# Optimization experiments

Measured on AMD Instinct MI355X. Metric: run time of the kernel, lower is better.

## Reference

```python
import jax, jax.numpy as jnp
import numpy as np

N_NODES = 100000
N_EDGES = 3200000


def setup_inputs() -> dict:
    key = jax.random.key(0)
    ks = jax.random.split(key, 12)
    x = jax.random.normal(ks[0], (N_NODES, 34), dtype=jnp.float32)
    edge_index = jax.random.randint(ks[1], (2, N_EDGES), 0, N_NODES, dtype=jnp.int64)
    def lin(k, fin, fout):
        s = 1.0 / np.sqrt(fin)
        kw, kb = jax.random.split(k)
        W = jax.random.uniform(kw, (fin, fout), jnp.float32, -s, s)
        b = jax.random.uniform(kb, (fout,), jnp.float32, -s, s)
        return W, b
    W1, b1 = lin(ks[2], 34, 64)
    W2, b2 = lin(ks[3], 64, 32)
    W3, b3 = lin(ks[4], 32, 16)
    W4, b4 = lin(ks[5], 16, 8)
    Wc, bc = lin(ks[6], 8, 2)
    return {"x": x, "edge_index": edge_index,
            "W1": W1, "b1": b1, "W2": W2, "b2": b2,
            "W3": W3, "b3": b3, "W4": W4, "b4": b4,
            "Wc": Wc, "bc": bc}


def _gcn_norm(edge_index, n_nodes):
    # PyG GCNConv: add self-loops, symmetric normalization D^-1/2 (A+I) D^-1/2
    loop = jnp.arange(n_nodes, dtype=edge_index.dtype)
    src = jnp.concatenate([edge_index[0], loop])  # [E+N]
    dst = jnp.concatenate([edge_index[1], loop])
    deg = jax.ops.segment_sum(jnp.ones_like(dst, dtype=jnp.float32), dst,
                              num_segments=n_nodes)
    dinv = jnp.where(deg > 0, jax.lax.rsqrt(deg), 0.0)
    norm = dinv[src] * dinv[dst]  # [E+N]
    return src, dst, norm


def _gcn_conv(h, W, b, src, dst, norm, n_nodes):
    h = h @ W                                    # [N, Fout] small GEMM
    msg = h[src] * norm[:, None]                 # gather + scale
    out = jax.ops.segment_sum(msg, dst, num_segments=n_nodes)  # scatter-add
    return out + b


def reference(x, edge_index, W1, b1, W2, b2, W3, b3, W4, b4, Wc, bc):
    n = x.shape[0]
    src, dst, norm = _gcn_norm(edge_index, n)
    h = jnp.tanh(_gcn_conv(x, W1, b1, src, dst, norm, n))
    h = jnp.tanh(_gcn_conv(h, W2, b2, src, dst, norm, n))
    h = jnp.tanh(_gcn_conv(h, W3, b3, src, dst, norm, n))
    h = jnp.tanh(_gcn_conv(h, W4, b4, src, dst, norm, n))
    out = h @ Wc + bc
    return (out, h)
```

## Files before the change

### kernel.cpp

```cpp
#include <hip/hip_runtime.h>
#include <math.h>

#define N_NODES 100000
#define BSHIFT 8
#define BNODES 256
#define NB ((N_NODES + BNODES - 1) / BNODES)
#define CHUNK 8192


typedef float f32x2 __attribute__((ext_vector_type(2)));

__device__ __forceinline__ unsigned short f2bf(float x) {
    unsigned u = __float_as_uint(x);
    u += 0x7FFFu + ((u >> 16) & 1u);
    return (unsigned short)(u >> 16);
}
__device__ __forceinline__ unsigned pack2(float a, float b) {
    return (unsigned)f2bf(a) | ((unsigned)f2bf(b) << 16);
}
__device__ __forceinline__ float bflo(unsigned u) { return __uint_as_float(u << 16); }
__device__ __forceinline__ float bfhi(unsigned u) { return __uint_as_float(u & 0xFFFF0000u); }

__device__ __forceinline__ int nt_ld(const int* p) { return __builtin_nontemporal_load(p); }
__device__ __forceinline__ void nt_st2(float* p, float a, float b) {
    f32x2 v; v.x = a; v.y = b;
    __builtin_nontemporal_store(v, (f32x2*)p);
}
__device__ __forceinline__ void nt_st(float* p, float a) { __builtin_nontemporal_store(a, p); }


__global__ __launch_bounds__(256) void bucket_count(const int* __restrict__ dst,
                                                    int* __restrict__ bucketCount, int E) {
    __shared__ int hist[NB];
    for (int i = threadIdx.x; i < NB; i += 256) hist[i] = 0;
    __syncthreads();
    int i = blockIdx.x * blockDim.x + threadIdx.x;
    int stride = gridDim.x * blockDim.x;
    for (int e = i; e < E; e += stride)
        atomicAdd(&hist[nt_ld(dst + e) >> BSHIFT], 1);
    __syncthreads();
    for (int i2 = threadIdx.x; i2 < NB; i2 += 256) {
        int c = hist[i2];
        if (c) atomicAdd(&bucketCount[i2], c);
    }
}


__global__ __launch_bounds__(512) void bucket_scan(const int* __restrict__ bucketCount,
                                                   int* __restrict__ bucketOff,
                                                   int* __restrict__ bucketCursor, int E) {
    __shared__ int sh[512];
    int t = threadIdx.x;
    int v = (t < NB) ? bucketCount[t] : 0;
    sh[t] = v;
    __syncthreads();
    for (int d = 1; d < 512; d <<= 1) {
        int u = (t >= d) ? sh[t - d] : 0;
        __syncthreads();
        sh[t] += u;
        __syncthreads();
    }
    if (t < NB) { bucketOff[t] = sh[t] - v; bucketCursor[t] = sh[t] - v; }
    if (t == 0) bucketOff[NB] = E;
}


__global__ __launch_bounds__(256) void bucket_fill(const int* __restrict__ src,
                                                   const int* __restrict__ dst,
                                                   int* __restrict__ bucketCursor,
                                                   unsigned int* __restrict__ binned, int E) {
    __shared__ int hist[NB];
    __shared__ int base[NB];
    __shared__ int lcur[NB];
    __shared__ unsigned int recs[CHUNK];
    __shared__ unsigned short bkt[CHUNK];
    int t = threadIdx.x;
    for (int i = t; i < NB; i += 256) { hist[i] = 0; lcur[i] = 0; }
    __syncthreads();
    int cbase = blockIdx.x * CHUNK;
#pragma unroll
    for (int j = 0; j < CHUNK / 256; ++j) {
        int slot = t + j * 256;
        int e = cbase + slot;
        if (e < E) {
            int s = nt_ld(src + e);
            int d = nt_ld(dst + e);
            recs[slot] = (unsigned)s | ((unsigned)(d & (BNODES - 1)) << 17);
            int b = d >> BSHIFT;
            bkt[slot] = (unsigned short)b;
            atomicAdd(&hist[b], 1);
        } else {
            bkt[slot] = 0xFFFF;
        }
    }
    __syncthreads();
    for (int i = t; i < NB; i += 256) {
        int c = hist[i];
        base[i] = c ? atomicAdd(&bucketCursor[i], c) : 0;
    }
    __syncthreads();
#pragma unroll
    for (int j = 0; j < CHUNK / 256; ++j) {
        int slot = t + j * 256;
        unsigned short b = bkt[slot];
        if (b != 0xFFFF) {
            int pos = base[b] + atomicAdd(&lcur[b], 1);
            binned[pos] = recs[slot];
        }
    }
}


__global__ __launch_bounds__(256) void node_off_sort(const unsigned int* __restrict__ binned,
                                                     const int* __restrict__ bucketOff,
                                                     int* __restrict__ off,
                                                     float* __restrict__ dinv,
                                                     int* __restrict__ srcs, int n, int E) {
    __shared__ int hist[BNODES];
    __shared__ int sh[BNODES];
    __shared__ int lcur[BNODES];
    int t = threadIdx.x;
    int b = blockIdx.x;
    hist[t] = 0;
    __syncthreads();
    int rb = bucketOff[b], re = bucketOff[b + 1];
    for (int e = rb + t; e < re; e += 256)
        atomicAdd(&hist[(binned[e] >> 17) & 255], 1);
    __syncthreads();
    int v = hist[t];
    sh[t] = v;
    __syncthreads();
    for (int d = 1; d < 256; d <<= 1) {
        int u = (t >= d) ? sh[t - d] : 0;
        __syncthreads();
        sh[t] += u;
        __syncthreads();
    }
    int base = rb + sh[t] - v;
    lcur[t] = base;
    int g = b * BNODES + t;
    if (g < n) {
        off[g] = base;
        dinv[g] = rsqrtf((float)v + 1.0f);
    }
    if (b == NB - 1 && t == 0) off[n] = E;
    __syncthreads();
    for (int e = rb + t; e < re; e += 256) {
        unsigned int r = binned[e];
        int pos = atomicAdd(&lcur[(r >> 17) & 255], 1);
        srcs[pos] = (int)(r & 0x1FFFF);
    }
}


__global__ void x_pack(const float* __restrict__ x, const float* __restrict__ dinv,
                       unsigned* __restrict__ xm, unsigned* __restrict__ xt, int n) {
    int i = blockIdx.x * blockDim.x + threadIdx.x;
    if (i >= n) return;
    float dv = dinv[i];
    const float2* xr = (const float2*)(x + (size_t)i * 34);
    unsigned* om = xm + (size_t)i * 16;
#pragma unroll
    for (int j = 0; j < 16; ++j) { float2 v = xr[j]; om[j] = pack2(dv * v.x, dv * v.y); }
    float2 v = xr[16];
    xt[i] = pack2(dv * v.x, dv * v.y);
}


__global__ __launch_bounds__(256) void gather_x_bf16(const int* __restrict__ off,
        const int* __restrict__ srcs, const unsigned* __restrict__ xm,
        const unsigned* __restrict__ xt, const float* __restrict__ dinv,
        float* __restrict__ aggx, int n) {
    int g = blockIdx.x * 16 + (threadIdx.x >> 4);
    int f = threadIdx.x & 15;
    if (g >= n) return;
    int rb = off[g], re = off[g + 1];
    unsigned ug = xm[(size_t)g * 16 + f];
    float a0 = bflo(ug), a1 = bfhi(ug);
    float a2 = 0.f, a3 = 0.f;
    if (f == 0) { unsigned tt = xt[g]; a2 = bflo(tt); a3 = bfhi(tt); }
    int e = rb;
    for (; e + 8 <= re; e += 8) {
        int s0 = nt_ld(srcs + e),     s1 = nt_ld(srcs + e + 1);
        int s2 = nt_ld(srcs + e + 2), s3 = nt_ld(srcs + e + 3);
        int s4 = nt_ld(srcs + e + 4), s5 = nt_ld(srcs + e + 5);
        int s6 = nt_ld(srcs + e + 6), s7 = nt_ld(srcs + e + 7);
        unsigned u0 = xm[(size_t)s0 * 16 + f], u1 = xm[(size_t)s1 * 16 + f];
        unsigned u2 = xm[(size_t)s2 * 16 + f], u3 = xm[(size_t)s3 * 16 + f];
        unsigned u4 = xm[(size_t)s4 * 16 + f], u5 = xm[(size_t)s5 * 16 + f];
        unsigned u6 = xm[(size_t)s6 * 16 + f], u7 = xm[(size_t)s7 * 16 + f];
        a0 += bflo(u0); a1 += bfhi(u0); a0 += bflo(u1); a1 += bfhi(u1);
        a0 += bflo(u2); a1 += bfhi(u2); a0 += bflo(u3); a1 += bfhi(u3);
        a0 += bflo(u4); a1 += bfhi(u4); a0 += bflo(u5); a1 += bfhi(u5);
        a0 += bflo(u6); a1 += bfhi(u6); a0 += bflo(u7); a1 += bfhi(u7);
        if (f == 0) {
            unsigned t0 = xt[s0], t1 = xt[s1], t2 = xt[s2], t3 = xt[s3];
            unsigned t4 = xt[s4], t5 = xt[s5], t6 = xt[s6], t7 = xt[s7];
            a2 += bflo(t0); a3 += bfhi(t0); a2 += bflo(t1); a3 += bfhi(t1);
            a2 += bflo(t2); a3 += bfhi(t2); a2 += bflo(t3); a3 += bfhi(t3);
            a2 += bflo(t4); a3 += bfhi(t4); a2 += bflo(t5); a3 += bfhi(t5);
            a2 += bflo(t6); a3 += bfhi(t6); a2 += bflo(t7); a3 += bfhi(t7);
        }
    }
    for (; e < re; ++e) {
        int s = nt_ld(srcs + e);
        unsigned u = xm[(size_t)s * 16 + f];
        a0 += bflo(u); a1 += bfhi(u);
        if (f == 0) { unsigned tt = xt[s]; a2 += bflo(tt); a3 += bfhi(tt); }
    }
    float dv = dinv[g];
    nt_st2(aggx + (size_t)g * 34 + 2 * f, dv * a0, dv * a1);
    if (f == 0) nt_st2(aggx + (size_t)g * 34 + 32, dv * a2, dv * a3);
}


template<int FIN, int FOUT>
__global__ void gemm_tanh(const float* __restrict__ h, const float* __restrict__ W,
                          const float* __restrict__ bias, float* __restrict__ o, int n) {
    __shared__ float sW[FIN * FOUT];
    for (int i = threadIdx.x; i < FIN * FOUT; i += blockDim.x) sW[i] = W[i];
    __syncthreads();
    constexpr int ROWS = 256 / FOUT;
    int f = threadIdx.x % FOUT;
    int r = threadIdx.x / FOUT;
    int row = blockIdx.x * ROWS + r;
    if (row >= n) return;
    const float* hr = h + (size_t)row * FIN;
    float acc = 0.f;
#pragma unroll
    for (int k = 0; k < FIN; ++k) acc = fmaf(hr[k], sW[k * FOUT + f], acc);
    nt_st(o + (size_t)row * FOUT + f, tanhf(acc + bias[f]));
}


template<int FIN, int FOUT>
__global__ void gemm_pack(const float* __restrict__ h, const float* __restrict__ W,
                          const float* __restrict__ dinv, unsigned* __restrict__ linh, int n) {
    __shared__ float sW[FIN * FOUT];
    for (int i = threadIdx.x; i < FIN * FOUT; i += blockDim.x) sW[i] = W[i];
    __syncthreads();
    constexpr int NL = FOUT / 2;
    constexpr int ROWS = 256 / NL;
    int f = threadIdx.x % NL;
    int r = threadIdx.x / NL;
    int row = blockIdx.x * ROWS + r;
    if (row >= n) return;
    const float* hr = h + (size_t)row * FIN;
    float a0 = 0.f, a1 = 0.f;
#pragma unroll
    for (int k = 0; k < FIN; ++k) {
        float v = hr[k];
        a0 = fmaf(v, sW[k * FOUT + 2 * f], a0);
        a1 = fmaf(v, sW[k * FOUT + 2 * f + 1], a1);
    }
    float dv = dinv[row];
    linh[(size_t)row * NL + f] = pack2(dv * a0, dv * a1);
}


template<int F, bool CLS>
__global__ __launch_bounds__(256) void gather_bf16(const int* __restrict__ off,
        const int* __restrict__ srcs, const unsigned* __restrict__ linh,
        const float* __restrict__ dinv, const float* __restrict__ bias,
        float* __restrict__ h, const float* __restrict__ Wc,
        const float* __restrict__ bc, float* __restrict__ out, int n) {
    constexpr int NL = F / 2;
    int g = blockIdx.x * (256 / NL) + threadIdx.x / NL;
    int f = threadIdx.x % NL;
    if (g >= n) return;
    int rb = off[g], re = off[g + 1];
    unsigned ug = linh[(size_t)g * NL + f];
    float a0 = bflo(ug), a1 = bfhi(ug);
    int e = rb;
    for (; e + 8 <= re; e += 8) {
        int s0 = nt_ld(srcs + e),     s1 = nt_ld(srcs + e + 1);
        int s2 = nt_ld(srcs + e + 2), s3 = nt_ld(srcs + e + 3);
        int s4 = nt_ld(srcs + e + 4), s5 = nt_ld(srcs + e + 5);
        int s6 = nt_ld(srcs + e + 6), s7 = nt_ld(srcs + e + 7);
        unsigned u0 = linh[(size_t)s0 * NL + f], u1 = linh[(size_t)s1 * NL + f];
        unsigned u2 = linh[(size_t)s2 * NL + f], u3 = linh[(size_t)s3 * NL + f];
        unsigned u4 = linh[(size_t)s4 * NL + f], u5 = linh[(size_t)s5 * NL + f];
        unsigned u6 = linh[(size_t)s6 * NL + f], u7 = linh[(size_t)s7 * NL + f];
        a0 += bflo(u0); a1 += bfhi(u0); a0 += bflo(u1); a1 += bfhi(u1);
        a0 += bflo(u2); a1 += bfhi(u2); a0 += bflo(u3); a1 += bfhi(u3);
        a0 += bflo(u4); a1 += bfhi(u4); a0 += bflo(u5); a1 += bfhi(u5);
        a0 += bflo(u6); a1 += bfhi(u6); a0 += bflo(u7); a1 += bfhi(u7);
    }
    for (; e < re; ++e) {
        int s = nt_ld(srcs + e);
        unsigned u = linh[(size_t)s * NL + f];
        a0 += bflo(u); a1 += bfhi(u);
    }
    float dv = dinv[g];
    a0 = tanhf(fmaf(dv, a0, bias[2 * f]));
    a1 = tanhf(fmaf(dv, a1, bias[2 * f + 1]));
    nt_st2(h + (size_t)g * F + 2 * f, a0, a1);
    if (CLS) {
        float p0 = a0 * Wc[4 * f]     + a1 * Wc[4 * f + 2];
        float p1 = a0 * Wc[4 * f + 1] + a1 * Wc[4 * f + 3];
        p0 += __shfl_xor(p0, 1); p1 += __shfl_xor(p1, 1);
        p0 += __shfl_xor(p0, 2); p1 += __shfl_xor(p1, 2);
        if (f == 0) {
            out[(size_t)g * 2]     = p0 + bc[0];
            out[(size_t)g * 2 + 1] = p1 + bc[1];
        }
    }
}


static inline char* alignp(char* p) {
    return (char*)(((uintptr_t)p + 15) & ~(uintptr_t)15);
}

extern "C" void kernel_launch(void* const* d_in, const int* in_sizes, int n_in,
                              void* d_out, int out_size, void* d_ws, size_t ws_size,
                              hipStream_t stream) {
    const float* x  = (const float*)d_in[0];
    const int*   ei = (const int*)d_in[1];
    const float* W1 = (const float*)d_in[2];  const float* b1 = (const float*)d_in[3];
    const float* W2 = (const float*)d_in[4];  const float* b2 = (const float*)d_in[5];
    const float* W3 = (const float*)d_in[6];  const float* b3 = (const float*)d_in[7];
    const float* W4 = (const float*)d_in[8];  const float* b4 = (const float*)d_in[9];
    const float* Wc = (const float*)d_in[10]; const float* bc = (const float*)d_in[11];

    float* out  = (float*)d_out;
    float* hout = out + (size_t)2 * N_NODES;

    const int n = N_NODES;
    const int E = in_sizes[1] / 2;
    const int* src = ei;
    const int* dst = ei + E;

    char* w = (char*)d_ws;
    float*        dinv         = (float*)w;        w = alignp(w + (size_t)n * 4);
    int*          bucketCount  = (int*)w;          w = alignp(w + (size_t)NB * 4);
    int*          bucketOff    = (int*)w;          w = alignp(w + (size_t)(NB + 1) * 4);
    int*          bucketCursor = (int*)w;          w = alignp(w + (size_t)NB * 4);
    int*          off          = (int*)w;          w = alignp(w + (size_t)(n + 1) * 4);
    unsigned int* binned       = (unsigned int*)w; w = alignp(w + (size_t)E * 4);
    int*          srcs         = (int*)w;          w = alignp(w + (size_t)E * 4);
    unsigned int* xm           = (unsigned int*)w; w = alignp(w + (size_t)n * 16 * 4);
    unsigned int* xt           = (unsigned int*)w; w = alignp(w + (size_t)n * 4);
    float*        aggx         = (float*)w;        w = alignp(w + (size_t)n * 34 * 4);
    float*        hA           = (float*)w;        w = alignp(w + (size_t)n * 64 * 4);
    float*        hB           = (float*)w;        w = alignp(w + (size_t)n * 32 * 4);
    unsigned int* linh         = (unsigned int*)w; w = alignp(w + (size_t)n * 16 * 4);

    hipMemsetAsync(bucketCount, 0, NB * sizeof(int), stream);
    bucket_count<<<1024, 256, 0, stream>>>(dst, bucketCount, E);
    bucket_scan<<<1, 512, 0, stream>>>(bucketCount, bucketOff, bucketCursor, E);
    bucket_fill<<<(E + CHUNK - 1) / CHUNK, 256, 0, stream>>>(src, dst, bucketCursor, binned, E);
    node_off_sort<<<NB, 256, 0, stream>>>(binned, bucketOff, off, dinv, srcs, n, E);
    x_pack<<<(n + 255) / 256, 256, 0, stream>>>(x, dinv, xm, xt, n);

    gather_x_bf16<<<(n + 15) / 16, 256, 0, stream>>>(off, srcs, xm, xt, dinv, aggx, n);
    gemm_tanh<34, 64><<<(n + 3) / 4, 256, 0, stream>>>(aggx, W1, b1, hA, n);

    gemm_pack<64, 32><<<(n + 15) / 16, 256, 0, stream>>>(hA, W2, dinv, linh, n);
    gather_bf16<32, false><<<(n + 15) / 16, 256, 0, stream>>>(off, srcs, linh, dinv, b2, hB,
                                                              Wc, bc, out, n);

    gemm_pack<32, 16><<<(n + 31) / 32, 256, 0, stream>>>(hB, W3, dinv, linh, n);
    gather_bf16<16, false><<<(n + 31) / 32, 256, 0, stream>>>(off, srcs, linh, dinv, b3, hA,
                                                              Wc, bc, out, n);

    gemm_pack<16, 8><<<(n + 63) / 64, 256, 0, stream>>>(hA, W4, dinv, linh, n);
    gather_bf16<8, true><<<(n + 63) / 64, 256, 0, stream>>>(off, srcs, linh, dinv, b4, hout,
                                                            Wc, bc, out, n);
}
```

Measured before the change: 510.9 us.

## Fuse layer GEMMs into neighboring gather kernels to cut intermediate round-trips

Merges the layer-1 GEMM+tanh with the layer-2 projection into one kernel that keeps the 64-wide hidden row in shared memory. Folds the layer-3 and layer-4 projections into the preceding gather kernels using wavefront shuffles to reduce across lanes. This removes three launches and the fp32 intermediate writes and reads of hA and hB. The cost is a 16-way shuffle reduction per node in gather2 and larger shared weight tiles. Nontemporal stores are also replaced by plain vector stores.

```diff
diff --git a/kernel.cpp b/kernel.cpp
--- a/kernel.cpp
+++ b/kernel.cpp
@@ -8,8 +8,6 @@
 #define CHUNK 8192
 
 
-typedef float f32x2 __attribute__((ext_vector_type(2)));
-
 __device__ __forceinline__ unsigned short f2bf(float x) {
     unsigned u = __float_as_uint(x);
     u += 0x7FFFu + ((u >> 16) & 1u);
@@ -20,13 +18,7 @@
 }
 __device__ __forceinline__ float bflo(unsigned u) { return __uint_as_float(u << 16); }
 __device__ __forceinline__ float bfhi(unsigned u) { return __uint_as_float(u & 0xFFFF0000u); }
-
 __device__ __forceinline__ int nt_ld(const int* p) { return __builtin_nontemporal_load(p); }
-__device__ __forceinline__ void nt_st2(float* p, float a, float b) {
-    f32x2 v; v.x = a; v.y = b;
-    __builtin_nontemporal_store(v, (f32x2*)p);
-}
-__device__ __forceinline__ void nt_st(float* p, float a) { __builtin_nontemporal_store(a, p); }
 
 
 __global__ __launch_bounds__(256) void bucket_count(const int* __restrict__ dst,
@@ -209,67 +201,60 @@
         if (f == 0) { unsigned tt = xt[s]; a2 += bflo(tt); a3 += bfhi(tt); }
     }
     float dv = dinv[g];
-    nt_st2(aggx + (size_t)g * 34 + 2 * f, dv * a0, dv * a1);
-    if (f == 0) nt_st2(aggx + (size_t)g * 34 + 32, dv * a2, dv * a3);
-}
-
-
-template<int FIN, int FOUT>
-__global__ void gemm_tanh(const float* __restrict__ h, const float* __restrict__ W,
-                          const float* __restrict__ bias, float* __restrict__ o, int n) {
-    __shared__ float sW[FIN * FOUT];
-    for (int i = threadIdx.x; i < FIN * FOUT; i += blockDim.x) sW[i] = W[i];
-    __syncthreads();
-    constexpr int ROWS = 256 / FOUT;
-    int f = threadIdx.x % FOUT;
-    int r = threadIdx.x / FOUT;
-    int row = blockIdx.x * ROWS + r;
-    if (row >= n) return;
-    const float* hr = h + (size_t)row * FIN;
-    float acc = 0.f;
-#pragma unroll
-    for (int k = 0; k < FIN; ++k) acc = fmaf(hr[k], sW[k * FOUT + f], acc);
-    nt_st(o + (size_t)row * FOUT + f, tanhf(acc + bias[f]));
-}
-
-
-template<int FIN, int FOUT>
-__global__ void gemm_pack(const float* __restrict__ h, const float* __restrict__ W,
-                          const float* __restrict__ dinv, unsigned* __restrict__ linh, int n) {
-    __shared__ float sW[FIN * FOUT];
-    for (int i = threadIdx.x; i < FIN * FOUT; i += blockDim.x) sW[i] = W[i];
-    __syncthreads();
-    constexpr int NL = FOUT / 2;
-    constexpr int ROWS = 256 / NL;
-    int f = threadIdx.x % NL;
-    int r = threadIdx.x / NL;
-    int row = blockIdx.x * ROWS + r;
-    if (row >= n) return;
-    const float* hr = h + (size_t)row * FIN;
-    float a0 = 0.f, a1 = 0.f;
-#pragma unroll
-    for (int k = 0; k < FIN; ++k) {
-        float v = hr[k];
-        a0 = fmaf(v, sW[k * FOUT + 2 * f], a0);
-        a1 = fmaf(v, sW[k * FOUT + 2 * f + 1], a1);
-    }
-    float dv = dinv[row];
-    linh[(size_t)row * NL + f] = pack2(dv * a0, dv * a1);
-}
-
-
-template<int F, bool CLS>
-__global__ __launch_bounds__(256) void gather_bf16(const int* __restrict__ off,
-        const int* __restrict__ srcs, const unsigned* __restrict__ linh,
-        const float* __restrict__ dinv, const float* __restrict__ bias,
-        float* __restrict__ h, const float* __restrict__ Wc,
-        const float* __restrict__ bc, float* __restrict__ out, int n) {
-    constexpr int NL = F / 2;
-    int g = blockIdx.x * (256 / NL) + threadIdx.x / NL;
-    int f = threadIdx.x % NL;
+    *(float2*)(aggx + (size_t)g * 34 + 2 * f) = make_float2(dv * a0, dv * a1);
+    if (f == 0) *(float2*)(aggx + (size_t)g * 34 + 32) = make_float2(dv * a2, dv * a3);
+}
+
+
+__global__ __launch_bounds__(256) void gemm12(const float* __restrict__ aggx,
+        const float* __restrict__ W1, const float* __restrict__ b1,
+        const float* __restrict__ W2, const float* __restrict__ dinv,
+        unsigned* __restrict__ linh2, int n) {
+    __shared__ float sW1[34 * 64];
+    __shared__ float sW2[64 * 32];
+    __shared__ float sh1[4][64];
+    for (int i = threadIdx.x; i < 34 * 64; i += 256) sW1[i] = W1[i];
+    for (int i = threadIdx.x; i < 64 * 32; i += 256) sW2[i] = W2[i];
+    __syncthreads();
+    int r = threadIdx.x / 64;
+    int j = threadIdx.x % 64;
+    int row = blockIdx.x * 4 + r;
+    float h1v = 0.f;
+    if (row < n) {
+        const float* hr = aggx + (size_t)row * 34;
+        float acc = 0.f;
+#pragma unroll
+        for (int k = 0; k < 34; ++k) acc = fmaf(hr[k], sW1[k * 64 + j], acc);
+        h1v = tanhf(acc + b1[j]);
+    }
+    sh1[r][j] = h1v;
+    __syncthreads();
+    if (row < n && j < 16) {
+        float a0 = 0.f, a1 = 0.f;
+#pragma unroll
+        for (int k = 0; k < 64; ++k) {
+            float v = sh1[r][k];
+            a0 = fmaf(v, sW2[k * 32 + 2 * j], a0);
+            a1 = fmaf(v, sW2[k * 32 + 2 * j + 1], a1);
+        }
+        float dv = dinv[row];
+        linh2[(size_t)row * 16 + j] = pack2(dv * a0, dv * a1);
+    }
+}
+
+
+__global__ __launch_bounds__(256) void gather2_proj(const int* __restrict__ off,
+        const int* __restrict__ srcs, const unsigned* __restrict__ linh2,
+        const float* __restrict__ dinv, const float* __restrict__ b2,
+        const float* __restrict__ W3, unsigned* __restrict__ linh3, int n) {
+    __shared__ float sW3[32 * 16];
+    for (int i = threadIdx.x; i < 32 * 16; i += 256) sW3[i] = W3[i];
+    __syncthreads();
+    int g = blockIdx.x * 16 + (threadIdx.x >> 4);
+    int f = threadIdx.x & 15;
     if (g >= n) return;
     int rb = off[g], re = off[g + 1];
-    unsigned ug = linh[(size_t)g * NL + f];
+    unsigned ug = linh2[(size_t)g * 16 + f];
     float a0 = bflo(ug), a1 = bfhi(ug);
     int e = rb;
     for (; e + 8 <= re; e += 8) {
@@ -277,10 +262,10 @@
         int s2 = nt_ld(srcs + e + 2), s3 = nt_ld(srcs + e + 3);
         int s4 = nt_ld(srcs + e + 4), s5 = nt_ld(srcs + e + 5);
         int s6 = nt_ld(srcs + e + 6), s7 = nt_ld(srcs + e + 7);
-        unsigned u0 = linh[(size_t)s0 * NL + f], u1 = linh[(size_t)s1 * NL + f];
-        unsigned u2 = linh[(size_t)s2 * NL + f], u3 = linh[(size_t)s3 * NL + f];
-        unsigned u4 = linh[(size_t)s4 * NL + f], u5 = linh[(size_t)s5 * NL + f];
-        unsigned u6 = linh[(size_t)s6 * NL + f], u7 = linh[(size_t)s7 * NL + f];
+        unsigned u0 = linh2[(size_t)s0 * 16 + f], u1 = linh2[(size_t)s1 * 16 + f];
+        unsigned u2 = linh2[(size_t)s2 * 16 + f], u3 = linh2[(size_t)s3 * 16 + f];
+        unsigned u4 = linh2[(size_t)s4 * 16 + f], u5 = linh2[(size_t)s5 * 16 + f];
+        unsigned u6 = linh2[(size_t)s6 * 16 + f], u7 = linh2[(size_t)s7 * 16 + f];
         a0 += bflo(u0); a1 += bfhi(u0); a0 += bflo(u1); a1 += bfhi(u1);
         a0 += bflo(u2); a1 += bfhi(u2); a0 += bflo(u3); a1 += bfhi(u3);
         a0 += bflo(u4); a1 += bfhi(u4); a0 += bflo(u5); a1 += bfhi(u5);
@@ -288,22 +273,114 @@
     }
     for (; e < re; ++e) {
         int s = nt_ld(srcs + e);
-        unsigned u = linh[(size_t)s * NL + f];
+        unsigned u = linh2[(size_t)s * 16 + f];
         a0 += bflo(u); a1 += bfhi(u);
     }
     float dv = dinv[g];
-    a0 = tanhf(fmaf(dv, a0, bias[2 * f]));
-    a1 = tanhf(fmaf(dv, a1, bias[2 * f + 1]));
-    nt_st2(h + (size_t)g * F + 2 * f, a0, a1);
-    if (CLS) {
-        float p0 = a0 * Wc[4 * f]     + a1 * Wc[4 * f + 2];
-        float p1 = a0 * Wc[4 * f + 1] + a1 * Wc[4 * f + 3];
-        p0 += __shfl_xor(p0, 1); p1 += __shfl_xor(p1, 1);
-        p0 += __shfl_xor(p0, 2); p1 += __shfl_xor(p1, 2);
-        if (f == 0) {
-            out[(size_t)g * 2]     = p0 + bc[0];
-            out[(size_t)g * 2 + 1] = p1 + bc[1];
-        }
+    float h0 = tanhf(fmaf(dv, a0, b2[2 * f]));
+    float h1 = tanhf(fmaf(dv, a1, b2[2 * f + 1]));
+    float p[16];
+#pragma unroll
+    for (int o = 0; o < 16; ++o)
+        p[o] = h0 * sW3[(2 * f) * 16 + o] + h1 * sW3[(2 * f + 1) * 16 + o];
+#pragma unroll
+    for (int m = 1; m <= 8; m <<= 1)
+#pragma unroll
+        for (int o = 0; o < 16; ++o) p[o] += __shfl_xor(p[o], m);
+    if (f < 8) linh3[(size_t)g * 8 + f] = pack2(dv * p[2 * f], dv * p[2 * f + 1]);
+}
+
+
+__global__ __launch_bounds__(256) void gather3_proj(const int* __restrict__ off,
+        const int* __restrict__ srcs, const unsigned* __restrict__ linh3,
+        const float* __restrict__ dinv, const float* __restrict__ b3,
+        const float* __restrict__ W4, unsigned* __restrict__ linh4, int n) {
+    __shared__ float sW4[16 * 8];
+    for (int i = threadIdx.x; i < 16 * 8; i += 256) sW4[i] = W4[i];
+    __syncthreads();
+    int g = blockIdx.x * 32 + (threadIdx.x >> 3);
+    int f = threadIdx.x & 7;
+    if (g >= n) return;
+    int rb = off[g], re = off[g + 1];
+    unsigned ug = linh3[(size_t)g * 8 + f];
+    float a0 = bflo(ug), a1 = bfhi(ug);
+    int e = rb;
+    for (; e + 8 <= re; e += 8) {
+        int s0 = nt_ld(srcs + e),     s1 = nt_ld(srcs + e + 1);
+        int s2 = nt_ld(srcs + e + 2), s3 = nt_ld(srcs + e + 3);
+        int s4 = nt_ld(srcs + e + 4), s5 = nt_ld(srcs + e + 5);
+        int s6 = nt_ld(srcs + e + 6), s7 = nt_ld(srcs + e + 7);
+        unsigned u0 = linh3[(size_t)s0 * 8 + f], u1 = linh3[(size_t)s1 * 8 + f];
+        unsigned u2 = linh3[(size_t)s2 * 8 + f], u3 = linh3[(size_t)s3 * 8 + f];
+        unsigned u4 = linh3[(size_t)s4 * 8 + f], u5 = linh3[(size_t)s5 * 8 + f];
+        unsigned u6 = linh3[(size_t)s6 * 8 + f], u7 = linh3[(size_t)s7 * 8 + f];
+        a0 += bflo(u0); a1 += bfhi(u0); a0 += bflo(u1); a1 += bfhi(u1);
+        a0 += bflo(u2); a1 += bfhi(u2); a0 += bflo(u3); a1 += bfhi(u3);
+        a0 += bflo(u4); a1 += bfhi(u4); a0 += bflo(u5); a1 += bfhi(u5);
+        a0 += bflo(u6); a1 += bfhi(u6); a0 += bflo(u7); a1 += bfhi(u7);
+    }
+    for (; e < re; ++e) {
+        int s = nt_ld(srcs + e);
+        unsigned u = linh3[(size_t)s * 8 + f];
+        a0 += bflo(u); a1 += bfhi(u);
+    }
+    float dv = dinv[g];
+    float h0 = tanhf(fmaf(dv, a0, b3[2 * f]));
+    float h1 = tanhf(fmaf(dv, a1, b3[2 * f + 1]));
+    float p[8];
+#pragma unroll
+    for (int o = 0; o < 8; ++o)
+        p[o] = h0 * sW4[(2 * f) * 8 + o] + h1 * sW4[(2 * f + 1) * 8 + o];
+#pragma unroll
+    for (int m = 1; m <= 4; m <<= 1)
+#pragma unroll
+        for (int o = 0; o < 8; ++o) p[o] += __shfl_xor(p[o], m);
+    if (f < 4) linh4[(size_t)g * 4 + f] = pack2(dv * p[2 * f], dv * p[2 * f + 1]);
+}
+
+
+__global__ __launch_bounds__(256) void gather4_cls(const int* __restrict__ off,
+        const int* __restrict__ srcs, const unsigned* __restrict__ linh4,
+        const float* __restrict__ dinv, const float* __restrict__ b4,
+        float* __restrict__ hout, const float* __restrict__ Wc,
+        const float* __restrict__ bc, float* __restrict__ out, int n) {
+    int g = blockIdx.x * 64 + (threadIdx.x >> 2);
+    int f = threadIdx.x & 3;
+    if (g >= n) return;
+    int rb = off[g], re = off[g + 1];
+    unsigned ug = linh4[(size_t)g * 4 + f];
+    float a0 = bflo(ug), a1 = bfhi(ug);
+    int e = rb;
+    for (; e + 8 <= re; e += 8) {
+        int s0 = nt_ld(srcs + e),     s1 = nt_ld(srcs + e + 1);
+        int s2 = nt_ld(srcs + e + 2), s3 = nt_ld(srcs + e + 3);
+        int s4 = nt_ld(srcs + e + 4), s5 = nt_ld(srcs + e + 5);
+        int s6 = nt_ld(srcs + e + 6), s7 = nt_ld(srcs + e + 7);
+        unsigned u0 = linh4[(size_t)s0 * 4 + f], u1 = linh4[(size_t)s1 * 4 + f];
+        unsigned u2 = linh4[(size_t)s2 * 4 + f], u3 = linh4[(size_t)s3 * 4 + f];
+        unsigned u4 = linh4[(size_t)s4 * 4 + f], u5 = linh4[(size_t)s5 * 4 + f];
+        unsigned u6 = linh4[(size_t)s6 * 4 + f], u7 = linh4[(size_t)s7 * 4 + f];
+        a0 += bflo(u0); a1 += bfhi(u0); a0 += bflo(u1); a1 += bfhi(u1);
+        a0 += bflo(u2); a1 += bfhi(u2); a0 += bflo(u3); a1 += bfhi(u3);
+        a0 += bflo(u4); a1 += bfhi(u4); a0 += bflo(u5); a1 += bfhi(u5);
+        a0 += bflo(u6); a1 += bfhi(u6); a0 += bflo(u7); a1 += bfhi(u7);
+    }
+    for (; e < re; ++e) {
+        int s = nt_ld(srcs + e);
+        unsigned u = linh4[(size_t)s * 4 + f];
+        a0 += bflo(u); a1 += bfhi(u);
+    }
+    float dv = dinv[g];
+    a0 = tanhf(fmaf(dv, a0, b4[2 * f]));
+    a1 = tanhf(fmaf(dv, a1, b4[2 * f + 1]));
+    *(float2*)(hout + (size_t)g * 8 + 2 * f) = make_float2(a0, a1);
+    float p0 = a0 * Wc[4 * f]     + a1 * Wc[4 * f + 2];
+    float p1 = a0 * Wc[4 * f + 1] + a1 * Wc[4 * f + 3];
+    p0 += __shfl_xor(p0, 1); p1 += __shfl_xor(p1, 1);
+    p0 += __shfl_xor(p0, 2); p1 += __shfl_xor(p1, 2);
+    if (f == 0) {
+        out[(size_t)g * 2]     = p0 + bc[0];
+        out[(size_t)g * 2 + 1] = p1 + bc[1];
     }
 }
 
@@ -318,7 +395,8 @@
     const float* x  = (const float*)d_in[0];
     const int*   ei = (const int*)d_in[1];
     const float* W1 = (const float*)d_in[2];  const float* b1 = (const float*)d_in[3];
-    const float* W2 = (const float*)d_in[4];  const float* b2 = (const float*)d_in[5];
+    const float* W2 = (const float*)d_in[4];
+    const float* b2 = (const float*)d_in[5];
     const float* W3 = (const float*)d_in[6];  const float* b3 = (const float*)d_in[7];
     const float* W4 = (const float*)d_in[8];  const float* b4 = (const float*)d_in[9];
     const float* Wc = (const float*)d_in[10]; const float* bc = (const float*)d_in[11];
@@ -342,9 +420,9 @@
     unsigned int* xm           = (unsigned int*)w; w = alignp(w + (size_t)n * 16 * 4);
     unsigned int* xt           = (unsigned int*)w; w = alignp(w + (size_t)n * 4);
     float*        aggx         = (float*)w;        w = alignp(w + (size_t)n * 34 * 4);
-    float*        hA           = (float*)w;        w = alignp(w + (size_t)n * 64 * 4);
-    float*        hB           = (float*)w;        w = alignp(w + (size_t)n * 32 * 4);
-    unsigned int* linh         = (unsigned int*)w; w = alignp(w + (size_t)n * 16 * 4);
+    unsigned int* linh2        = (unsigned int*)w; w = alignp(w + (size_t)n * 16 * 4);
+    unsigned int* linh3        = (unsigned int*)w; w = alignp(w + (size_t)n * 8 * 4);
+    unsigned int* linh4        = (unsigned int*)w; w = alignp(w + (size_t)n * 4 * 4);
 
     hipMemsetAsync(bucketCount, 0, NB * sizeof(int), stream);
     bucket_count<<<1024, 256, 0, stream>>>(dst, bucketCount, E);
@@ -354,17 +432,12 @@
     x_pack<<<(n + 255) / 256, 256, 0, stream>>>(x, dinv, xm, xt, n);
 
     gather_x_bf16<<<(n + 15) / 16, 256, 0, stream>>>(off, srcs, xm, xt, dinv, aggx, n);
-    gemm_tanh<34, 64><<<(n + 3) / 4, 256, 0, stream>>>(aggx, W1, b1, hA, n);
-
-    gemm_pack<64, 32><<<(n + 15) / 16, 256, 0, stream>>>(hA, W2, dinv, linh, n);
-    gather_bf16<32, false><<<(n + 15) / 16, 256, 0, stream>>>(off, srcs, linh, dinv, b2, hB,
-                                                              Wc, bc, out, n);
-
-    gemm_pack<32, 16><<<(n + 31) / 32, 256, 0, stream>>>(hB, W3, dinv, linh, n);
-    gather_bf16<16, false><<<(n + 31) / 32, 256, 0, stream>>>(off, srcs, linh, dinv, b3, hA,
-                                                              Wc, bc, out, n);
-
-    gemm_pack<16, 8><<<(n + 63) / 64, 256, 0, stream>>>(hA, W4, dinv, linh, n);
-    gather_bf16<8, true><<<(n + 63) / 64, 256, 0, stream>>>(off, srcs, linh, dinv, b4, hout,
-                                                            Wc, bc, out, n);
-}
+    gemm12<<<(n + 3) / 4, 256, 0, stream>>>(aggx, W1, b1, W2, dinv, linh2, n);
+
+    gather2_proj<<<(n + 15) / 16, 256, 0, stream>>>(off, srcs, linh2, dinv, b2, W3, linh3, n);
+
+    gather3_proj<<<(n + 31) / 32, 256, 0, stream>>>(off, srcs, linh3, dinv, b3, W4, linh4, n);
+
+    gather4_cls<<<(n + 63) / 64, 256, 0, stream>>>(off, srcs, linh4, dinv, b4, hout,
+                                                   Wc, bc, out, n);
+}
```

After: 507.8 us. No clear change (-0.6%).
